# Kernel optimization log

Hardware: AMD Instinct MI355X
Metric: run time of the kernel (lower is better)

Reference implementation:

```python
import jax, jax.numpy as jnp
import numpy as np

BITS = 2
GROUP_SIZE = 128
EPS = 1e-8


def fake_quant(w):
    """Per-group (contiguous 128-element, over flattened weight) min/max fake quantization."""
    max_q = (1 << BITS) - 1  # 3 for INT2
    flat = w.reshape(-1, GROUP_SIZE)            # [num_groups, group_size]
    mn = flat.min(axis=1, keepdims=True)
    mx = flat.max(axis=1, keepdims=True)
    rng = mx - mn
    scale = rng / max_q
    safe_scale = jnp.where(rng < EPS, 1.0, scale)  # avoid div-by-zero
    q = jnp.clip(jnp.round((flat - mn) / safe_scale), 0, max_q)
    deq = q * scale + mn
    out = jnp.where(rng < EPS, flat, deq)        # pass-through for near-constant groups
    return out.reshape(w.shape)


def setup_inputs() -> dict:
    key = jax.random.key(0)
    kx, kw, kb = jax.random.split(key, 3)
    B, S, D_IN, D_OUT = 4, 2048, 4096, 4096
    x = jax.random.normal(kx, (B, S, D_IN), dtype=jnp.float32)
    # kaiming-uniform-like init scale
    bound = float(np.sqrt(6.0 / D_IN))
    weight = jax.random.uniform(kw, (D_OUT, D_IN), minval=-bound, maxval=bound, dtype=jnp.float32)
    bias = jnp.zeros((D_OUT,), dtype=jnp.float32)
    return {"x": x, "weight": weight, "bias": bias}


def reference(x, weight, bias):
    # training-mode forward: STE fake-quant of weight, then linear
    w_quant = weight + jax.lax.stop_gradient(fake_quant(weight) - weight)
    return jnp.einsum('bsd,od->bso', x, w_quant) + bias
```

## Files before the change

kernel.cpp:

```cpp
#include <hip/hip_runtime.h>
#include <hip/hip_bf16.h>
#include <stdint.h>

#define M_DIM 8192
#define N_DIM 4096
#define K_DIM 4096

typedef __hip_bfloat16 bf16;
typedef __attribute__((ext_vector_type(8))) short bf16x8;
typedef __attribute__((ext_vector_type(4))) float floatx4;

typedef const uint32_t GQ __attribute__((address_space(1)));
typedef uint32_t LQ __attribute__((address_space(3)));

__device__ __forceinline__ uint2 pack_bf16x4(float4 v) {
  bf16 b0 = __float2bfloat16(v.x);
  bf16 b1 = __float2bfloat16(v.y);
  bf16 b2 = __float2bfloat16(v.z);
  bf16 b3 = __float2bfloat16(v.w);
  unsigned int lo = (unsigned int)*(unsigned short*)&b0 |
                    ((unsigned int)*(unsigned short*)&b1 << 16);
  unsigned int hi = (unsigned int)*(unsigned short*)&b2 |
                    ((unsigned int)*(unsigned short*)&b3 << 16);
  return make_uint2(lo, hi);
}

__global__ void quant_w_kernel(const float* __restrict__ w, bf16* __restrict__ wq) {
  const int t = blockIdx.x * blockDim.x + threadIdx.x;
  const int g = t >> 4;
  const int s = t & 15;

  const float4* p = (const float4*)(w + (size_t)g * 128);
  float4 a = p[s];
  float4 b = p[s + 16];

  float mn = fminf(fminf(fminf(a.x, a.y), fminf(a.z, a.w)),
                   fminf(fminf(b.x, b.y), fminf(b.z, b.w)));
  float mx = fmaxf(fmaxf(fmaxf(a.x, a.y), fmaxf(a.z, a.w)),
                   fmaxf(fmaxf(b.x, b.y), fmaxf(b.z, b.w)));
#pragma unroll
  for (int off = 8; off >= 1; off >>= 1) {
    mn = fminf(mn, __shfl_xor(mn, off));
    mx = fmaxf(mx, __shfl_xor(mx, off));
  }
  const float rng = mx - mn;
  float4 oa, ob;
  if (rng < 1e-8f) {
    oa = a; ob = b;
  } else {
    const float scale = rng / 3.0f;
    float q0 = fminf(fmaxf(rintf((a.x - mn) / scale), 0.f), 3.f);
    float q1 = fminf(fmaxf(rintf((a.y - mn) / scale), 0.f), 3.f);
    float q2 = fminf(fmaxf(rintf((a.z - mn) / scale), 0.f), 3.f);
    float q3 = fminf(fmaxf(rintf((a.w - mn) / scale), 0.f), 3.f);
    float q4 = fminf(fmaxf(rintf((b.x - mn) / scale), 0.f), 3.f);
    float q5 = fminf(fmaxf(rintf((b.y - mn) / scale), 0.f), 3.f);
    float q6 = fminf(fmaxf(rintf((b.z - mn) / scale), 0.f), 3.f);
    float q7 = fminf(fmaxf(rintf((b.w - mn) / scale), 0.f), 3.f);
    oa = make_float4(q0 * scale + mn, q1 * scale + mn, q2 * scale + mn, q3 * scale + mn);
    ob = make_float4(q4 * scale + mn, q5 * scale + mn, q6 * scale + mn, q7 * scale + mn);
  }
  uint2* q = (uint2*)(wq + (size_t)g * 128);
  q[s]      = pack_bf16x4(oa);
  q[s + 16] = pack_bf16x4(ob);
}

__global__ void cast_x_kernel(const float* __restrict__ x, bf16* __restrict__ xb) {
  const size_t base = (size_t)blockIdx.x * 512;
  const int tid = threadIdx.x;
  const float4* p = (const float4*)x + base;
  float4 a = p[tid];
  float4 b = p[tid + 256];
  uint2* q = (uint2*)xb + base;
  q[tid]       = pack_bf16x4(a);
  q[tid + 256] = pack_bf16x4(b);
}

#define BM 256
#define BN 256
#define BK 64
#define NT (K_DIM / BK)

#define MFMA_BF16 __builtin_amdgcn_mfma_f32_16x16x32_bf16

__device__ __forceinline__ bf16x8 lds_read_b128(const bf16* p) {
  bf16x8 r;
  asm volatile("ds_read_b128 %0, %1" : "=v"(r) : "v"((const LQ*)p));
  return r;
}

__device__ __forceinline__ void stage_tile(const bf16* __restrict__ Ag,
                                           const bf16* __restrict__ Bg,
                                           bf16* sa, bf16* sb,
                                           int k0, int warp, int lane) {
  const int srow = warp * 8 + (lane >> 3);
  const int scol = ((lane & 7) ^ ((lane >> 3) & 7)) * 8;
#pragma unroll
  for (int j = 0; j < 4; ++j) {
    const bf16* g = Ag + (size_t)(j * 64 + srow) * K_DIM + (k0 + scol);
    bf16* l = sa + (j * 64 + warp * 8) * BK;
    __builtin_amdgcn_global_load_lds((GQ*)g, (LQ*)l, 16, 0, 0);
  }
#pragma unroll
  for (int j = 0; j < 4; ++j) {
    const bf16* g = Bg + (size_t)(j * 64 + srow) * K_DIM + (k0 + scol);
    bf16* l = sb + (j * 64 + warp * 8) * BK;
    __builtin_amdgcn_global_load_lds((GQ*)g, (LQ*)l, 16, 0, 0);
  }
}

#define PHASE_WAIT()                                    \
  __builtin_amdgcn_s_barrier();                         \
  __builtin_amdgcn_sched_barrier(0);                    \
  asm volatile("s_waitcnt lgkmcnt(0)" ::: "memory");    \
  __builtin_amdgcn_sched_barrier(0);                    \
  __builtin_amdgcn_s_setprio(1)

#define PHASE_CLOSE()                                   \
  __builtin_amdgcn_s_setprio(0);                        \
  __builtin_amdgcn_sched_barrier(0);                    \
  __builtin_amdgcn_s_barrier();                         \
  __builtin_amdgcn_sched_barrier(0)

__device__ __forceinline__ void do_ktile(const bf16* sa, const bf16* sb,
                                         floatx4 (&acc)[8][4],
                                         const int aBase, const int bBase,
                                         const int c0, const int c1) {
  bf16x8 af[4][2];
  bf16x8 bfr[2][2];

#pragma unroll
  for (int i = 0; i < 4; ++i) {
    af[i][0] = lds_read_b128(sa + aBase + i * 16 * BK + c0);
    af[i][1] = lds_read_b128(sa + aBase + i * 16 * BK + c1);
  }
#pragma unroll
  for (int j = 0; j < 2; ++j) {
    bfr[j][0] = lds_read_b128(sb + bBase + j * 16 * BK + c0);
    bfr[j][1] = lds_read_b128(sb + bBase + j * 16 * BK + c1);
  }
  PHASE_WAIT();
#pragma unroll
  for (int s = 0; s < 2; ++s)
#pragma unroll
    for (int i = 0; i < 4; ++i)
#pragma unroll
      for (int j = 0; j < 2; ++j)
        acc[i][j] = MFMA_BF16(af[i][s], bfr[j][s], acc[i][j], 0, 0, 0);
  PHASE_CLOSE();

#pragma unroll
  for (int j = 0; j < 2; ++j) {
    bfr[j][0] = lds_read_b128(sb + bBase + (2 + j) * 16 * BK + c0);
    bfr[j][1] = lds_read_b128(sb + bBase + (2 + j) * 16 * BK + c1);
  }
  PHASE_WAIT();
#pragma unroll
  for (int s = 0; s < 2; ++s)
#pragma unroll
    for (int i = 0; i < 4; ++i)
#pragma unroll
      for (int j = 0; j < 2; ++j)
        acc[i][2 + j] = MFMA_BF16(af[i][s], bfr[j][s], acc[i][2 + j], 0, 0, 0);
  PHASE_CLOSE();

#pragma unroll
  for (int i = 0; i < 4; ++i) {
    af[i][0] = lds_read_b128(sa + aBase + (4 + i) * 16 * BK + c0);
    af[i][1] = lds_read_b128(sa + aBase + (4 + i) * 16 * BK + c1);
  }
  PHASE_WAIT();
#pragma unroll
  for (int s = 0; s < 2; ++s)
#pragma unroll
    for (int i = 0; i < 4; ++i)
#pragma unroll
      for (int j = 0; j < 2; ++j)
        acc[4 + i][2 + j] = MFMA_BF16(af[i][s], bfr[j][s], acc[4 + i][2 + j], 0, 0, 0);
  PHASE_CLOSE();

#pragma unroll
  for (int j = 0; j < 2; ++j) {
    bfr[j][0] = lds_read_b128(sb + bBase + j * 16 * BK + c0);
    bfr[j][1] = lds_read_b128(sb + bBase + j * 16 * BK + c1);
  }
  PHASE_WAIT();
#pragma unroll
  for (int s = 0; s < 2; ++s)
#pragma unroll
    for (int i = 0; i < 4; ++i)
#pragma unroll
      for (int j = 0; j < 2; ++j)
        acc[4 + i][j] = MFMA_BF16(af[i][s], bfr[j][s], acc[4 + i][j], 0, 0, 0);
  PHASE_CLOSE();
}

__global__ __launch_bounds__(512, 2)
void gemm_bt_kernel(const bf16* __restrict__ A,
                    const bf16* __restrict__ Bw,
                    const float* __restrict__ bias,
                    float* __restrict__ C) {
  extern __shared__ bf16 smem[];
  bf16* sA0 = smem;
  bf16* sB0 = smem + 1 * BM * BK;
  bf16* sA1 = smem + 2 * BM * BK;
  bf16* sB1 = smem + 3 * BM * BK;

  const int tid  = threadIdx.x;
  const int lane = tid & 63;
  const int warp = tid >> 6;
  const int wm   = warp >> 2;
  const int wn   = warp & 3;
  const int m0   = blockIdx.y * BM;
  const int n0   = blockIdx.x * BN;

  const bf16* Ag = A  + (size_t)m0 * K_DIM;
  const bf16* Bg = Bw + (size_t)n0 * K_DIM;

  floatx4 acc[8][4];
#pragma unroll
  for (int i = 0; i < 8; ++i)
#pragma unroll
    for (int j = 0; j < 4; ++j)
      acc[i][j] = (floatx4){0.f, 0.f, 0.f, 0.f};

  const int fr = lane & 15;
  const int fs = lane & 7;
  const int fc = lane >> 4;
  const int c0 = ((0 + fc) ^ fs) * 8;
  const int c1 = ((4 + fc) ^ fs) * 8;
  const int aBase = (wm * 128 + fr) * BK;
  const int bBase = (wn * 64 + fr) * BK;

  stage_tile(Ag, Bg, sA0, sB0, 0 * BK, warp, lane);
  stage_tile(Ag, Bg, sA1, sB1, 1 * BK, warp, lane);
  asm volatile("s_waitcnt vmcnt(8)" ::: "memory");
  __builtin_amdgcn_s_barrier();
  __builtin_amdgcn_sched_barrier(0);

#pragma unroll 1
  for (int tt = 0; tt < NT; tt += 2) {
    do_ktile(sA0, sB0, acc, aBase, bBase, c0, c1);
    if (tt + 2 < NT) {
      stage_tile(Ag, Bg, sA0, sB0, (tt + 2) * BK, warp, lane);
      asm volatile("s_waitcnt vmcnt(8)" ::: "memory");
    } else {
      asm volatile("s_waitcnt vmcnt(0)" ::: "memory");
    }
    __builtin_amdgcn_s_barrier();
    __builtin_amdgcn_sched_barrier(0);

    do_ktile(sA1, sB1, acc, aBase, bBase, c0, c1);
    if (tt + 3 < NT) {
      stage_tile(Ag, Bg, sA1, sB1, (tt + 3) * BK, warp, lane);
      asm volatile("s_waitcnt vmcnt(8)" ::: "memory");
      __builtin_amdgcn_s_barrier();
      __builtin_amdgcn_sched_barrier(0);
    }
  }

  const int cm = (lane >> 4) * 4;
  const int cn = lane & 15;
#pragma unroll
  for (int j = 0; j < 4; ++j) {
    const int col = n0 + wn * 64 + j * 16 + cn;
    const float bv = bias[col];
#pragma unroll
    for (int i = 0; i < 8; ++i) {
      const int rowb = m0 + wm * 128 + i * 16 + cm;
      float* outp = C + (size_t)rowb * N_DIM + col;
#pragma unroll
      for (int r = 0; r < 4; ++r)
        outp[(size_t)r * N_DIM] = acc[i][j][r] + bv;
    }
  }
}

extern "C" void kernel_launch(void* const* d_in, const int* in_sizes, int n_in,
                              void* d_out, int out_size, void* d_ws, size_t ws_size,
                              hipStream_t stream) {
  const float* x      = (const float*)d_in[0];
  const float* weight = (const float*)d_in[1];
  const float* bias   = (const float*)d_in[2];
  float* out          = (float*)d_out;

  bf16* wq = (bf16*)d_ws;
  bf16* xb = (bf16*)((char*)d_ws + (size_t)N_DIM * K_DIM * sizeof(bf16));

  {
    int threads = (N_DIM * K_DIM) / 8;
    quant_w_kernel<<<threads / 256, 256, 0, stream>>>(weight, wq);
  }
  {
    int threads = (M_DIM * K_DIM) / 8;
    cast_x_kernel<<<threads / 256, 256, 0, stream>>>(x, xb);
  }
  {
    constexpr int smem_bytes = 4 * BM * BK * (int)sizeof(bf16);
    static bool attr_done = false;
    if (!attr_done) {
      (void)hipFuncSetAttribute((const void*)gemm_bt_kernel,
                                hipFuncAttributeMaxDynamicSharedMemorySize,
                                smem_bytes);
      attr_done = true;
    }
    dim3 grid(N_DIM / BN, M_DIM / BM);
    gemm_bt_kernel<<<grid, 512, smem_bytes, stream>>>(xb, wq, bias, out);
  }
}
```

Baseline: 520.4 us.

## Split LDS tiles into halves and interleave half-tile prefetch with MFMA phases

Splits the A and B LDS tiles into two halves each, remapping rows so each warp's fragments live in one half. Global-to-LDS loads for the next tiles are issued in pieces between the four MFMA phases, as each half is freed, instead of as one block after the whole k-tile. The barrier before each MFMA phase is dropped, leaving one vmcnt wait and barrier per tile. This aims to keep memory traffic overlapped with compute and cut barrier stalls, but the buffer-reuse ordering is intricate and a mistake would race.

```diff
diff --git a/kernel.cpp b/kernel.cpp
--- a/kernel.cpp
+++ b/kernel.cpp
@@ -80,6 +80,7 @@
 #define BN 256
 #define BK 64
 #define NT (K_DIM / BK)
+#define HALF 8192
 
 #define MFMA_BF16 __builtin_amdgcn_mfma_f32_16x16x32_bf16
 
@@ -89,29 +90,36 @@
   return r;
 }
 
-__device__ __forceinline__ void stage_tile(const bf16* __restrict__ Ag,
-                                           const bf16* __restrict__ Bg,
-                                           bf16* sa, bf16* sb,
-                                           int k0, int warp, int lane) {
-  const int srow = warp * 8 + (lane >> 3);
+__device__ __forceinline__ void stage_A_half(const bf16* __restrict__ Ag,
+                                             bf16* lds_half, int k0, int hA,
+                                             int warp, int lane) {
+  const int sub  = warp * 8 + (lane >> 3);
   const int scol = ((lane & 7) ^ ((lane >> 3) & 7)) * 8;
 #pragma unroll
-  for (int j = 0; j < 4; ++j) {
-    const bf16* g = Ag + (size_t)(j * 64 + srow) * K_DIM + (k0 + scol);
-    bf16* l = sa + (j * 64 + warp * 8) * BK;
+  for (int i = 0; i < 2; ++i) {
+    const int r = (sub & 63) + hA * 64 + i * 128;
+    const bf16* g = Ag + (size_t)r * K_DIM + (k0 + scol);
+    bf16* l = lds_half + (i * 64 + warp * 8) * BK;
     __builtin_amdgcn_global_load_lds((GQ*)g, (LQ*)l, 16, 0, 0);
   }
-#pragma unroll
-  for (int j = 0; j < 4; ++j) {
-    const bf16* g = Bg + (size_t)(j * 64 + srow) * K_DIM + (k0 + scol);
-    bf16* l = sb + (j * 64 + warp * 8) * BK;
+}
+
+__device__ __forceinline__ void stage_B_half(const bf16* __restrict__ Bg,
+                                             bf16* lds_half, int k0, int hB,
+                                             int warp, int lane) {
+  const int sub  = warp * 8 + (lane >> 3);
+  const int scol = ((lane & 7) ^ ((lane >> 3) & 7)) * 8;
+#pragma unroll
+  for (int i = 0; i < 2; ++i) {
+    const int idx = i * 64 + sub;
+    const int r = (idx & 31) + hB * 32 + (idx >> 5) * 64;
+    const bf16* g = Bg + (size_t)r * K_DIM + (k0 + scol);
+    bf16* l = lds_half + (i * 64 + warp * 8) * BK;
     __builtin_amdgcn_global_load_lds((GQ*)g, (LQ*)l, 16, 0, 0);
   }
 }
 
-#define PHASE_WAIT()                                    \
-  __builtin_amdgcn_s_barrier();                         \
-  __builtin_amdgcn_sched_barrier(0);                    \
+#define PHASE_MFMA_OPEN()                               \
   asm volatile("s_waitcnt lgkmcnt(0)" ::: "memory");    \
   __builtin_amdgcn_sched_barrier(0);                    \
   __builtin_amdgcn_s_setprio(1)
@@ -122,77 +130,85 @@
   __builtin_amdgcn_s_barrier();                         \
   __builtin_amdgcn_sched_barrier(0)
 
-__device__ __forceinline__ void do_ktile(const bf16* sa, const bf16* sb,
-                                         floatx4 (&acc)[8][4],
-                                         const int aBase, const int bBase,
-                                         const int c0, const int c1) {
+__device__ __forceinline__ void do_tile(const bf16* cA, const bf16* cB, bf16* nA,
+                                        const bf16* __restrict__ Ag,
+                                        const bf16* __restrict__ Bg,
+                                        int k1, int k2, int g1, int g2,
+                                        int warp, int lane,
+                                        int aoff, int boff, int c0, int c1,
+                                        floatx4 (&acc)[8][4]) {
   bf16x8 af[4][2];
-  bf16x8 bfr[2][2];
+  bf16x8 bl[2][2];
+  bf16x8 bh[2][2];
 
 #pragma unroll
   for (int i = 0; i < 4; ++i) {
-    af[i][0] = lds_read_b128(sa + aBase + i * 16 * BK + c0);
-    af[i][1] = lds_read_b128(sa + aBase + i * 16 * BK + c1);
+    af[i][0] = lds_read_b128(cA + aoff + i * 16 * BK + c0);
+    af[i][1] = lds_read_b128(cA + aoff + i * 16 * BK + c1);
   }
 #pragma unroll
   for (int j = 0; j < 2; ++j) {
-    bfr[j][0] = lds_read_b128(sb + bBase + j * 16 * BK + c0);
-    bfr[j][1] = lds_read_b128(sb + bBase + j * 16 * BK + c1);
-  }
-  PHASE_WAIT();
+    bl[j][0] = lds_read_b128(cB + boff + j * 16 * BK + c0);
+    bl[j][1] = lds_read_b128(cB + boff + j * 16 * BK + c1);
+  }
+  if (g1) stage_A_half(Ag, nA + HALF, k1, 1, warp, lane);
+  PHASE_MFMA_OPEN();
 #pragma unroll
   for (int s = 0; s < 2; ++s)
 #pragma unroll
     for (int i = 0; i < 4; ++i)
 #pragma unroll
       for (int j = 0; j < 2; ++j)
-        acc[i][j] = MFMA_BF16(af[i][s], bfr[j][s], acc[i][j], 0, 0, 0);
+        acc[i][j] = MFMA_BF16(af[i][s], bl[j][s], acc[i][j], 0, 0, 0);
   PHASE_CLOSE();
 
 #pragma unroll
   for (int j = 0; j < 2; ++j) {
-    bfr[j][0] = lds_read_b128(sb + bBase + (2 + j) * 16 * BK + c0);
-    bfr[j][1] = lds_read_b128(sb + bBase + (2 + j) * 16 * BK + c1);
-  }
-  PHASE_WAIT();
+    bh[j][0] = lds_read_b128(cB + HALF + boff + j * 16 * BK + c0);
+    bh[j][1] = lds_read_b128(cB + HALF + boff + j * 16 * BK + c1);
+  }
+  if (g2) stage_A_half(Ag, (bf16*)cA, k2, 0, warp, lane);
+  PHASE_MFMA_OPEN();
 #pragma unroll
   for (int s = 0; s < 2; ++s)
 #pragma unroll
     for (int i = 0; i < 4; ++i)
 #pragma unroll
       for (int j = 0; j < 2; ++j)
-        acc[i][2 + j] = MFMA_BF16(af[i][s], bfr[j][s], acc[i][2 + j], 0, 0, 0);
+        acc[i][2 + j] = MFMA_BF16(af[i][s], bh[j][s], acc[i][2 + j], 0, 0, 0);
   PHASE_CLOSE();
 
 #pragma unroll
   for (int i = 0; i < 4; ++i) {
-    af[i][0] = lds_read_b128(sa + aBase + (4 + i) * 16 * BK + c0);
-    af[i][1] = lds_read_b128(sa + aBase + (4 + i) * 16 * BK + c1);
-  }
-  PHASE_WAIT();
+    af[i][0] = lds_read_b128(cA + HALF + aoff + i * 16 * BK + c0);
+    af[i][1] = lds_read_b128(cA + HALF + aoff + i * 16 * BK + c1);
+  }
+  if (g2) stage_B_half(Bg, (bf16*)cB, k2, 0, warp, lane);
+  PHASE_MFMA_OPEN();
 #pragma unroll
   for (int s = 0; s < 2; ++s)
 #pragma unroll
     for (int i = 0; i < 4; ++i)
 #pragma unroll
       for (int j = 0; j < 2; ++j)
-        acc[4 + i][2 + j] = MFMA_BF16(af[i][s], bfr[j][s], acc[4 + i][2 + j], 0, 0, 0);
+        acc[4 + i][2 + j] = MFMA_BF16(af[i][s], bh[j][s], acc[4 + i][2 + j], 0, 0, 0);
   PHASE_CLOSE();
 
-#pragma unroll
-  for (int j = 0; j < 2; ++j) {
-    bfr[j][0] = lds_read_b128(sb + bBase + j * 16 * BK + c0);
-    bfr[j][1] = lds_read_b128(sb + bBase + j * 16 * BK + c1);
-  }
-  PHASE_WAIT();
+  if (g2) stage_B_half(Bg, (bf16*)cB + HALF, k2, 1, warp, lane);
+  __builtin_amdgcn_s_setprio(1);
 #pragma unroll
   for (int s = 0; s < 2; ++s)
 #pragma unroll
     for (int i = 0; i < 4; ++i)
 #pragma unroll
       for (int j = 0; j < 2; ++j)
-        acc[4 + i][j] = MFMA_BF16(af[i][s], bfr[j][s], acc[4 + i][j], 0, 0, 0);
-  PHASE_CLOSE();
+        acc[4 + i][j] = MFMA_BF16(af[i][s], bl[j][s], acc[4 + i][j], 0, 0, 0);
+  __builtin_amdgcn_s_setprio(0);
+  __builtin_amdgcn_sched_barrier(0);
+  if (g2) { asm volatile("s_waitcnt vmcnt(6)" ::: "memory"); }
+  else    { asm volatile("s_waitcnt vmcnt(0)" ::: "memory"); }
+  __builtin_amdgcn_s_barrier();
+  __builtin_amdgcn_sched_barrier(0);
 }
 
 __global__ __launch_bounds__(512, 2)
@@ -202,9 +218,9 @@
                     float* __restrict__ C) {
   extern __shared__ bf16 smem[];
   bf16* sA0 = smem;
-  bf16* sB0 = smem + 1 * BM * BK;
-  bf16* sA1 = smem + 2 * BM * BK;
-  bf16* sB1 = smem + 3 * BM * BK;
+  bf16* sB0 = smem + 16384;
+  bf16* sA1 = smem + 32768;
+  bf16* sB1 = smem + 49152;
 
   const int tid  = threadIdx.x;
   const int lane = tid & 63;
@@ -229,34 +245,26 @@
   const int fc = lane >> 4;
   const int c0 = ((0 + fc) ^ fs) * 8;
   const int c1 = ((4 + fc) ^ fs) * 8;
-  const int aBase = (wm * 128 + fr) * BK;
-  const int bBase = (wn * 64 + fr) * BK;
-
-  stage_tile(Ag, Bg, sA0, sB0, 0 * BK, warp, lane);
-  stage_tile(Ag, Bg, sA1, sB1, 1 * BK, warp, lane);
-  asm volatile("s_waitcnt vmcnt(8)" ::: "memory");
+  const int aoff = (wm * 64 + fr) * BK;
+  const int boff = (wn * 32 + fr) * BK;
+
+  stage_A_half(Ag, sA0,        0,  0, warp, lane);
+  stage_B_half(Bg, sB0,        0,  0, warp, lane);
+  stage_B_half(Bg, sB0 + HALF, 0,  1, warp, lane);
+  stage_A_half(Ag, sA0 + HALF, 0,  1, warp, lane);
+  stage_A_half(Ag, sA1,        BK, 0, warp, lane);
+  stage_B_half(Bg, sB1,        BK, 0, warp, lane);
+  stage_B_half(Bg, sB1 + HALF, BK, 1, warp, lane);
+  asm volatile("s_waitcnt vmcnt(6)" ::: "memory");
   __builtin_amdgcn_s_barrier();
   __builtin_amdgcn_sched_barrier(0);
 
 #pragma unroll 1
-  for (int tt = 0; tt < NT; tt += 2) {
-    do_ktile(sA0, sB0, acc, aBase, bBase, c0, c1);
-    if (tt + 2 < NT) {
-      stage_tile(Ag, Bg, sA0, sB0, (tt + 2) * BK, warp, lane);
-      asm volatile("s_waitcnt vmcnt(8)" ::: "memory");
-    } else {
-      asm volatile("s_waitcnt vmcnt(0)" ::: "memory");
-    }
-    __builtin_amdgcn_s_barrier();
-    __builtin_amdgcn_sched_barrier(0);
-
-    do_ktile(sA1, sB1, acc, aBase, bBase, c0, c1);
-    if (tt + 3 < NT) {
-      stage_tile(Ag, Bg, sA1, sB1, (tt + 3) * BK, warp, lane);
-      asm volatile("s_waitcnt vmcnt(8)" ::: "memory");
-      __builtin_amdgcn_s_barrier();
-      __builtin_amdgcn_sched_barrier(0);
-    }
+  for (int u = 0; u < NT; u += 2) {
+    do_tile(sA0, sB0, sA1, Ag, Bg, (u + 1) * BK, (u + 2) * BK,
+            (u + 1) < NT, (u + 2) < NT, warp, lane, aoff, boff, c0, c1, acc);
+    do_tile(sA1, sB1, sA0, Ag, Bg, (u + 2) * BK, (u + 3) * BK,
+            (u + 2) < NT, (u + 3) < NT, warp, lane, aoff, boff, c0, c1, acc);
   }
 
   const int cm = (lane >> 4) * 4;
```

New measurement: 486.0 us. -6.6%, faster.
